# Optimization experiments

Measured on AMD Instinct MI355X. Metric: run time of the kernel, lower is better.

## Reference

```python
import jax, jax.numpy as jnp
import numpy as np

B, C, H, W = 8, 256, 64, 64


def setup_inputs() -> dict:
    key = jax.random.key(0)
    ks = jax.random.split(key, 6)
    s = 0.02
    return {
        "x": jax.random.normal(ks[0], (B, C, H, W), dtype=jnp.float32),
        "w_theta": jax.random.normal(ks[1], (C // 8, C), dtype=jnp.float32) * s,
        "b_theta": jnp.zeros((C // 8,), dtype=jnp.float32),
        "w_phi": jax.random.normal(ks[2], (C // 8, C), dtype=jnp.float32) * s,
        "b_phi": jnp.zeros((C // 8,), dtype=jnp.float32),
        "w_g": jax.random.normal(ks[3], (C // 2, C), dtype=jnp.float32) * s,
        "b_g": jnp.zeros((C // 2,), dtype=jnp.float32),
        "w_o": jax.random.normal(ks[4], (C, C // 2), dtype=jnp.float32) * s,
        "b_o": jnp.zeros((C,), dtype=jnp.float32),
        "gamma": jnp.zeros((1,), dtype=jnp.float32),
    }


def _conv1x1(x, w, b):
    # x: [B,Cin,H,W], w: [Cout,Cin] -> [B,Cout,H,W]
    return jnp.einsum('bchw,oc->bohw', x, w) + b[None, :, None, None]


def _maxpool2(t):
    b, c, h, w = t.shape
    return t.reshape(b, c, h // 2, 2, w // 2, 2).max(axis=(3, 5))


def reference(x, w_theta, b_theta, w_phi, b_phi, w_g, b_g, w_o, b_o, gamma):
    b, c, h, w = x.shape
    theta = _conv1x1(x, w_theta, b_theta).reshape(b, c // 8, h * w)      # [B,C/8,HW]
    phi = _maxpool2(_conv1x1(x, w_phi, b_phi)).reshape(b, c // 8, h * w // 4)  # [B,C/8,HW/4]
    attn = jax.nn.softmax(jnp.einsum('bcn,bcm->bnm', theta, phi), axis=-1)    # [B,HW,HW/4]
    g = _maxpool2(_conv1x1(x, w_g, b_g)).reshape(b, c // 2, h * w // 4)       # [B,C/2,HW/4]
    o = jnp.einsum('bcm,bnm->bcn', g, attn).reshape(b, c // 2, h, w)          # [B,C/2,H,W]
    o = _conv1x1(o, w_o, b_o)
    return gamma * o + x
```

## Files before the change

kernel.cpp:

```cpp
#include <hip/hip_runtime.h>
#include <cstdint>
#include <cstddef>

#define BATCH 8
#define CIN   256
#define CK    32
#define CV    128
#define HW_   4096
#define HWP   1024

typedef __attribute__((ext_vector_type(8))) short bf16x8;
typedef __attribute__((ext_vector_type(4))) float f32x4;
typedef __attribute__((ext_vector_type(4))) short short4v;

__device__ __forceinline__ short f2bf(float f) {
    union { float f; unsigned u; } v; v.f = f;
    unsigned r = v.u + 0x7fffu + ((v.u >> 16) & 1u);
    return (short)(r >> 16);
}
__device__ __forceinline__ float bf2f(short s) {
    union { unsigned u; float f; } v; v.u = ((unsigned)(unsigned short)s) << 16;
    return v.f;
}

#define WCAT_OFF 0u
#define WO_OFF   98304u
#define BCAT_OFF 163840u
#define XT_OFF   164864u
#define THT_OFF  16942080u
#define PHIT_OFF 19039232u
#define GP_OFF   19563520u

__global__ void prep_kernel(const float* __restrict__ wt, const float* __restrict__ bt,
                            const float* __restrict__ wp, const float* __restrict__ bp,
                            const float* __restrict__ wg, const float* __restrict__ bg,
                            const float* __restrict__ wo,
                            short* __restrict__ wcat_b, float* __restrict__ bcat,
                            short* __restrict__ wo_b) {
    int idx = blockIdx.x * 256 + threadIdx.x;
    if (idx < 192 * 256) {
        int o = idx >> 8, c = idx & 255;
        float v;
        if (o < 32)      v = wt[o * CIN + c];
        else if (o < 64) v = wp[(o - 32) * CIN + c];
        else             v = wg[(o - 64) * CIN + c];
        wcat_b[idx] = f2bf(v);
    } else {
        int i2 = idx - 192 * 256;
        wo_b[i2] = f2bf(wo[i2]);
    }
    if (blockIdx.x == 0 && threadIdx.x < 192) {
        int o = threadIdx.x;
        bcat[o] = (o < 32) ? bt[o] : (o < 64) ? bp[o - 32] : bg[o - 64];
    }
}

__global__ void __launch_bounds__(256) xt_kernel(const float* __restrict__ x,
                                                 short* __restrict__ x_t) {
    __shared__ float xs[64][65];
    int blk = blockIdx.x;
    int b = blk >> 8, rem = blk & 255, cblk = rem >> 6, nblk = rem & 63;
    int t = threadIdx.x;
#pragma unroll
    for (int i = 0; i < 16; ++i) {
        int idx = t + i * 256, c = idx >> 6, n = idx & 63;
        xs[c][n] = x[((size_t)(b * CIN + cblk * 64 + c)) * HW_ + nblk * 64 + n];
    }
    __syncthreads();
#pragma unroll
    for (int i = 0; i < 16; ++i) {
        int idx = t + i * 256, n = idx >> 6, c = idx & 63;
        x_t[((size_t)(b * HW_ + nblk * 64 + n)) * CIN + cblk * 64 + c] = f2bf(xs[c][n]);
    }
}

__global__ void __launch_bounds__(512) proj_pool_kernel(const short* __restrict__ x_t,
                                                        const short* __restrict__ wcat_b,
                                                        const float* __restrict__ bcat,
                                                        short* __restrict__ theta_t,
                                                        short* __restrict__ phi_t,
                                                        short* __restrict__ g_p) {
    __shared__ __align__(16) char smem[65536];
    int id = blockIdx.x;
    int b = id >> 5, rp = id & 31;
    int n0 = rp * 128;
    int t = threadIdx.x, l = t & 63, w = t >> 6, l15 = l & 15, lg = l >> 4;

#pragma unroll
    for (int i = 0; i < 8; ++i) {
        int chunk = t + i * 512, n = chunk >> 5, cc = chunk & 31;
        bf16x8 v = *(const bf16x8*)(x_t + ((size_t)(b * HW_ + n0 + n)) * CIN + cc * 8);
        *(bf16x8*)(smem + n * 512 + ((cc * 16) ^ ((n & 7) << 4))) = v;
    }
    __syncthreads();

    int og = w >> 1, nh = w & 1;
    f32x4 acc[3][4];
#pragma unroll
    for (int a = 0; a < 3; ++a)
#pragma unroll
        for (int nt = 0; nt < 4; ++nt) acc[a][nt] = (f32x4)0.f;

    for (int kk = 0; kk < 8; ++kk) {
        bf16x8 ao[3], bn[4];
#pragma unroll
        for (int oi = 0; oi < 3; ++oi) {
            int orow = og * 48 + oi * 16 + l15;
            ao[oi] = *(const bf16x8*)(wcat_b + orow * CIN + kk * 32 + lg * 8);
        }
#pragma unroll
        for (int nt = 0; nt < 4; ++nt) {
            int nr = nh * 64 + nt * 16 + l15;
            bn[nt] = *(const bf16x8*)(smem + nr * 512 + ((kk * 64 + lg * 16) ^ ((nr & 7) << 4)));
        }
#pragma unroll
        for (int oi = 0; oi < 3; ++oi)
#pragma unroll
            for (int nt = 0; nt < 4; ++nt)
                acc[oi][nt] = __builtin_amdgcn_mfma_f32_16x16x32_bf16(ao[oi], bn[nt], acc[oi][nt], 0, 0, 0);
    }
    __syncthreads();

#pragma unroll
    for (int oi = 0; oi < 3; ++oi)
#pragma unroll
        for (int nt = 0; nt < 4; ++nt)
#pragma unroll
            for (int r = 0; r < 4; ++r) {
                int o = og * 48 + oi * 16 + lg * 4 + r;
                int n = nh * 64 + nt * 16 + l15;
                float val = acc[oi][nt][r] + bcat[o];
                if (o < 32) val *= 1.44269504f;
                *(short*)(smem + n * 384 + ((o * 2) ^ ((n & 7) << 4))) = f2bf(val);
            }
    __syncthreads();

    {
        int n = t >> 2, cc = t & 3;
        bf16x8 v = *(const bf16x8*)(smem + n * 384 + ((cc * 16) ^ ((n & 7) << 4)));
        *(bf16x8*)(theta_t + ((size_t)(b * HW_ + n0 + n)) * CK + cc * 8) = v;
    }
#pragma unroll
    for (int jj = 0; jj < 2; ++jj) {
        int idx = t + jj * 512, wp = idx >> 5, c = idx & 31, o = 32 + c;
        int na = 2 * wp, nb2 = 2 * wp + 1;
        float v0 = bf2f(*(const short*)(smem + na * 384 + ((o * 2) ^ ((na & 7) << 4))));
        float v1 = bf2f(*(const short*)(smem + nb2 * 384 + ((o * 2) ^ ((nb2 & 7) << 4))));
        float v2 = bf2f(*(const short*)(smem + (64 + na) * 384 + ((o * 2) ^ (((64 + na) & 7) << 4))));
        float v3 = bf2f(*(const short*)(smem + (64 + nb2) * 384 + ((o * 2) ^ (((64 + nb2) & 7) << 4))));
        phi_t[((size_t)(b * HWP + rp * 32 + wp)) * CK + c] = f2bf(fmaxf(fmaxf(v0, v1), fmaxf(v2, v3)));
    }
#pragma unroll
    for (int jj = 0; jj < 8; ++jj) {
        int idx = t + jj * 512, cv = idx >> 5, wp = idx & 31, o = 64 + cv;
        int na = 2 * wp, nb2 = 2 * wp + 1;
        float v0 = bf2f(*(const short*)(smem + na * 384 + ((o * 2) ^ ((na & 7) << 4))));
        float v1 = bf2f(*(const short*)(smem + nb2 * 384 + ((o * 2) ^ ((nb2 & 7) << 4))));
        float v2 = bf2f(*(const short*)(smem + (64 + na) * 384 + ((o * 2) ^ (((64 + na) & 7) << 4))));
        float v3 = bf2f(*(const short*)(smem + (64 + nb2) * 384 + ((o * 2) ^ (((64 + nb2) & 7) << 4))));
        g_p[((size_t)(b * CV + cv)) * HWP + rp * 32 + wp] = f2bf(fmaxf(fmaxf(v0, v1), fmaxf(v2, v3)));
    }
}

#define PHI_PITCH 80
#define APHI0 0
#define AG0   5120
#define APHI1 21504
#define AG1   26624
#define AP    43008
#define ALS   51200
#define ALINV 52224
#define AO    0

__global__ void __launch_bounds__(256) attn_out_kernel(const short* __restrict__ theta_t,
                                                       const short* __restrict__ phi_t,
                                                       const short* __restrict__ g_p,
                                                       const short* __restrict__ wo_b,
                                                       const float* __restrict__ b_o,
                                                       const float* __restrict__ gamma,
                                                       const float* __restrict__ x,
                                                       float* __restrict__ out) {
    __shared__ __align__(16) char smem[52480];
    int id = blockIdx.x;
    int b = id & 7, q = id >> 3;
    int n0 = q * 64;
    int t = threadIdx.x, w = t >> 6, l = t & 63, l15 = l & 15, lg = l >> 4;

    bf16x8 qb[4];
#pragma unroll
    for (int nt = 0; nt < 4; ++nt)
        qb[nt] = *(const bf16x8*)(theta_t + ((size_t)(b * HW_ + n0 + nt * 16 + l15)) * CK + lg * 8);

    f32x4 oacc[8];
#pragma unroll
    for (int i = 0; i < 8; ++i) oacc[i] = (f32x4)0.f;
    float l_part[4] = {0.f, 0.f, 0.f, 0.f};

    const int sphioff = (t >> 2) * PHI_PITCH + (t & 3) * 16;
    const short* phisrc = phi_t + ((size_t)(b * HWP + (t >> 2))) * CK + (t & 3) * 8;
    const int mc = t & 7, cvb = t >> 3;
    const short* gs0 = g_p + ((size_t)(b * CV + cvb)) * HWP + mc * 8;
    const short* gs1 = gs0 + (size_t)32 * HWP;
    const short* gs2 = gs0 + (size_t)64 * HWP;
    const short* gs3 = gs0 + (size_t)96 * HWP;
    const int sg0 = cvb * 128 + ((mc * 16) ^ ((cvb & 7) << 4));
    const int sg1 = (cvb + 32) * 128 + ((mc * 16) ^ (((cvb + 32) & 7) << 4));
    const int sg2 = (cvb + 64) * 128 + ((mc * 16) ^ (((cvb + 64) & 7) << 4));
    const int sg3 = (cvb + 96) * 128 + ((mc * 16) ^ (((cvb + 96) & 7) << 4));

    bf16x8 pphi = *(const bf16x8*)phisrc;
    bf16x8 pg0 = *(const bf16x8*)gs0, pg1 = *(const bf16x8*)gs1;
    bf16x8 pg2 = *(const bf16x8*)gs2, pg3 = *(const bf16x8*)gs3;
    *(bf16x8*)(smem + APHI0 + sphioff) = pphi;
    *(bf16x8*)(smem + AG0 + sg0) = pg0;
    *(bf16x8*)(smem + AG0 + sg1) = pg1;
    *(bf16x8*)(smem + AG0 + sg2) = pg2;
    *(bf16x8*)(smem + AG0 + sg3) = pg3;
    __syncthreads();

    for (int kt = 0; kt < 16; ++kt) {
        const int cur = kt & 1;
        const int sb_phi = cur ? APHI1 : APHI0;
        const int sb_g   = cur ? AG1 : AG0;
        if (kt < 15) {
            phisrc += 64 * CK; gs0 += 64; gs1 += 64; gs2 += 64; gs3 += 64;
            pphi = *(const bf16x8*)phisrc;
            pg0 = *(const bf16x8*)gs0; pg1 = *(const bf16x8*)gs1;
            pg2 = *(const bf16x8*)gs2; pg3 = *(const bf16x8*)gs3;
        }
        bf16x8 pa = *(const bf16x8*)(smem + sb_phi + (w * 16 + l15) * PHI_PITCH + lg * 16);
        f32x4 sacc[4];
#pragma unroll
        for (int nt = 0; nt < 4; ++nt)
            sacc[nt] = __builtin_amdgcn_mfma_f32_16x16x32_bf16(pa, qb[nt], (f32x4)0.f, 0, 0, 0);
#pragma unroll
        for (int nt = 0; nt < 4; ++nt) {
            float p0 = __builtin_amdgcn_exp2f(sacc[nt][0]);
            float p1 = __builtin_amdgcn_exp2f(sacc[nt][1]);
            float p2 = __builtin_amdgcn_exp2f(sacc[nt][2]);
            float p3 = __builtin_amdgcn_exp2f(sacc[nt][3]);
            l_part[nt] += (p0 + p1) + (p2 + p3);
            short4v pk;
            pk[0] = f2bf(p0); pk[1] = f2bf(p1); pk[2] = f2bf(p2); pk[3] = f2bf(p3);
            int n = nt * 16 + l15;
            *(short4v*)(smem + AP + n * 128 + ((w * 32 + lg * 8) ^ ((n & 7) << 4))) = pk;
        }
        __syncthreads();

#pragma unroll
        for (int ks = 0; ks < 2; ++ks) {
            int np = w * 16 + l15;
            bf16x8 pva = *(const bf16x8*)(smem + AP + np * 128 + ((ks * 64 + lg * 16) ^ ((np & 7) << 4)));
#pragma unroll
            for (int cvt = 0; cvt < 8; ++cvt) {
                int cv = cvt * 16 + l15;
                bf16x8 gb = *(const bf16x8*)(smem + sb_g + cv * 128 + ((ks * 64 + lg * 16) ^ ((cv & 7) << 4)));
                oacc[cvt] = __builtin_amdgcn_mfma_f32_16x16x32_bf16(pva, gb, oacc[cvt], 0, 0, 0);
            }
        }
        if (kt < 15) {
            const int nb_phi = cur ? APHI0 : APHI1;
            const int nb_g   = cur ? AG0 : AG1;
            *(bf16x8*)(smem + nb_phi + sphioff) = pphi;
            *(bf16x8*)(smem + nb_g + sg0) = pg0;
            *(bf16x8*)(smem + nb_g + sg1) = pg1;
            *(bf16x8*)(smem + nb_g + sg2) = pg2;
            *(bf16x8*)(smem + nb_g + sg3) = pg3;
        }
        __syncthreads();
    }

#pragma unroll
    for (int nt = 0; nt < 4; ++nt) {
        l_part[nt] += __shfl_xor(l_part[nt], 16);
        l_part[nt] += __shfl_xor(l_part[nt], 32);
    }
    if (lg == 0) {
#pragma unroll
        for (int nt = 0; nt < 4; ++nt)
            *(float*)(smem + ALS + (nt * 16 + l15) * 16 + w * 4) = l_part[nt];
    }
    __syncthreads();
    if (t < 64) {
        f32x4 s4 = *(const f32x4*)(smem + ALS + t * 16);
        *(float*)(smem + ALINV + t * 4) = 1.f / ((s4[0] + s4[1]) + (s4[2] + s4[3]));
    }
    __syncthreads();
    f32x4 linv = *(const f32x4*)(smem + ALINV + (w * 16 + lg * 4) * 4);

#pragma unroll
    for (int cvt = 0; cvt < 8; ++cvt)
#pragma unroll
        for (int r = 0; r < 4; ++r) {
            int n = w * 16 + lg * 4 + r, cv = cvt * 16 + l15;
            *(short*)(smem + AO + n * 256 + ((cv * 2) ^ ((n & 7) << 4))) = f2bf(oacc[cvt][r] * linv[r]);
        }
    __syncthreads();

    f32x4 acc2[4][4];
#pragma unroll
    for (int a = 0; a < 4; ++a)
#pragma unroll
        for (int nt = 0; nt < 4; ++nt) acc2[a][nt] = (f32x4)0.f;

    for (int kk = 0; kk < 4; ++kk) {
        bf16x8 wa[4], ob[4];
#pragma unroll
        for (int ot = 0; ot < 4; ++ot) {
            int orow = w * 64 + ot * 16 + l15;
            wa[ot] = *(const bf16x8*)(wo_b + orow * CV + kk * 32 + lg * 8);
        }
#pragma unroll
        for (int nt = 0; nt < 4; ++nt) {
            int nl = nt * 16 + l15;
            ob[nt] = *(const bf16x8*)(smem + AO + nl * 256 + ((kk * 64 + lg * 16) ^ ((nl & 7) << 4)));
        }
#pragma unroll
        for (int ot = 0; ot < 4; ++ot)
#pragma unroll
            for (int nt = 0; nt < 4; ++nt)
                acc2[ot][nt] = __builtin_amdgcn_mfma_f32_16x16x32_bf16(wa[ot], ob[nt], acc2[ot][nt], 0, 0, 0);
    }

    float gm = gamma[0];
#pragma unroll
    for (int ot = 0; ot < 4; ++ot)
#pragma unroll
        for (int r = 0; r < 4; ++r) {
            int o = w * 64 + ot * 16 + lg * 4 + r;
            float bo = b_o[o];
#pragma unroll
            for (int nt = 0; nt < 4; ++nt) {
                size_t idx = ((size_t)(b * CIN + o)) * HW_ + n0 + nt * 16 + l15;
                out[idx] = fmaf(gm, acc2[ot][nt][r] + bo, x[idx]);
            }
        }
}

extern "C" void kernel_launch(void* const* d_in, const int* in_sizes, int n_in,
                              void* d_out, int out_size, void* d_ws, size_t ws_size,
                              hipStream_t stream) {
    const float* x       = (const float*)d_in[0];
    const float* w_theta = (const float*)d_in[1];
    const float* b_theta = (const float*)d_in[2];
    const float* w_phi   = (const float*)d_in[3];
    const float* b_phi   = (const float*)d_in[4];
    const float* w_g     = (const float*)d_in[5];
    const float* b_g     = (const float*)d_in[6];
    const float* w_o     = (const float*)d_in[7];
    const float* b_o     = (const float*)d_in[8];
    const float* gamma   = (const float*)d_in[9];
    float* out = (float*)d_out;
    char* wsb = (char*)d_ws;

    short* wcat_b  = (short*)(wsb + WCAT_OFF);
    short* wo_b    = (short*)(wsb + WO_OFF);
    float* bcat    = (float*)(wsb + BCAT_OFF);
    short* x_t     = (short*)(wsb + XT_OFF);
    short* theta_t = (short*)(wsb + THT_OFF);
    short* phi_t   = (short*)(wsb + PHIT_OFF);
    short* g_p     = (short*)(wsb + GP_OFF);

    prep_kernel<<<dim3(320), dim3(256), 0, stream>>>(w_theta, b_theta, w_phi, b_phi,
                                                     w_g, b_g, w_o, wcat_b, bcat, wo_b);
    xt_kernel<<<dim3(2048), dim3(256), 0, stream>>>(x, x_t);
    proj_pool_kernel<<<dim3(256), dim3(512), 0, stream>>>(x_t, wcat_b, bcat,
                                                          theta_t, phi_t, g_p);
    attn_out_kernel<<<dim3(512), dim3(256), 0, stream>>>(theta_t, phi_t, g_p, wo_b,
                                                         b_o, gamma, x, out);
}
```

Before: 146.1 us.

## Fuse x transpose/bf16 conversion into projection kernel with double-buffered fp32 staging

Removes the separate xt_kernel, which transposed x into an HW-major bf16 workspace. The projection kernel now reads fp32 x directly in 32-channel slices and stages them in a swizzled, double-buffered LDS tile, prefetching the next slice into registers while the current one is used. It converts to bf16 while building the MFMA B operand. This drops one kernel launch and an 16 MB write plus read round trip. In exchange it adds scalar LDS reads and per-element conversion in the inner loop, and a barrier on every k-step.

```diff
diff --git a/kernel.cpp b/kernel.cpp
--- a/kernel.cpp
+++ b/kernel.cpp
@@ -26,7 +26,6 @@
 #define WCAT_OFF 0u
 #define WO_OFF   98304u
 #define BCAT_OFF 163840u
-#define XT_OFF   164864u
 #define THT_OFF  16942080u
 #define PHIT_OFF 19039232u
 #define GP_OFF   19563520u
@@ -55,43 +54,30 @@
     }
 }
 
-__global__ void __launch_bounds__(256) xt_kernel(const float* __restrict__ x,
-                                                 short* __restrict__ x_t) {
-    __shared__ float xs[64][65];
-    int blk = blockIdx.x;
-    int b = blk >> 8, rem = blk & 255, cblk = rem >> 6, nblk = rem & 63;
-    int t = threadIdx.x;
-#pragma unroll
-    for (int i = 0; i < 16; ++i) {
-        int idx = t + i * 256, c = idx >> 6, n = idx & 63;
-        xs[c][n] = x[((size_t)(b * CIN + cblk * 64 + c)) * HW_ + nblk * 64 + n];
-    }
-    __syncthreads();
-#pragma unroll
-    for (int i = 0; i < 16; ++i) {
-        int idx = t + i * 256, n = idx >> 6, c = idx & 63;
-        x_t[((size_t)(b * HW_ + nblk * 64 + n)) * CIN + cblk * 64 + c] = f2bf(xs[c][n]);
-    }
-}
-
-__global__ void __launch_bounds__(512) proj_pool_kernel(const short* __restrict__ x_t,
+#define XS_PITCH 528
+#define XS_SZ    16896
+__global__ void __launch_bounds__(512) proj_pool_kernel(const float* __restrict__ x,
                                                         const short* __restrict__ wcat_b,
                                                         const float* __restrict__ bcat,
                                                         short* __restrict__ theta_t,
                                                         short* __restrict__ phi_t,
                                                         short* __restrict__ g_p) {
-    __shared__ __align__(16) char smem[65536];
+    __shared__ __align__(16) char smem[49152];
     int id = blockIdx.x;
     int b = id >> 5, rp = id & 31;
     int n0 = rp * 128;
     int t = threadIdx.x, l = t & 63, w = t >> 6, l15 = l & 15, lg = l >> 4;
 
-#pragma unroll
-    for (int i = 0; i < 8; ++i) {
-        int chunk = t + i * 512, n = chunk >> 5, cc = chunk & 31;
-        bf16x8 v = *(const bf16x8*)(x_t + ((size_t)(b * HW_ + n0 + n)) * CIN + cc * 8);
-        *(bf16x8*)(smem + n * 512 + ((cc * 16) ^ ((n & 7) << 4))) = v;
-    }
+    const int cl = t >> 4, nb = (t & 15) * 8;
+    const int swz_w = ((cl >> 3) & 3) << 5;
+    const int wo0 = cl * XS_PITCH + ((nb * 4) ^ swz_w);
+    const int wo1 = cl * XS_PITCH + (((nb + 4) * 4) ^ swz_w);
+    const float* xsrc = x + ((size_t)(b * CIN + cl) * HW_ + n0 + nb);
+
+    f32x4 sa = *(const f32x4*)(xsrc);
+    f32x4 sb = *(const f32x4*)(xsrc + 4);
+    *(f32x4*)(smem + wo0) = sa;
+    *(f32x4*)(smem + wo1) = sb;
     __syncthreads();
 
     int og = w >> 1, nh = w & 1;
@@ -102,24 +88,42 @@
         for (int nt = 0; nt < 4; ++nt) acc[a][nt] = (f32x4)0.f;
 
     for (int kk = 0; kk < 8; ++kk) {
+        const int cur = kk & 1;
+        if (kk < 7) {
+            const float* nsrc = xsrc + (size_t)(kk + 1) * 32 * HW_;
+            sa = *(const f32x4*)(nsrc);
+            sb = *(const f32x4*)(nsrc + 4);
+        }
         bf16x8 ao[3], bn[4];
 #pragma unroll
         for (int oi = 0; oi < 3; ++oi) {
             int orow = og * 48 + oi * 16 + l15;
             ao[oi] = *(const bf16x8*)(wcat_b + orow * CIN + kk * 32 + lg * 8);
         }
-#pragma unroll
-        for (int nt = 0; nt < 4; ++nt) {
-            int nr = nh * 64 + nt * 16 + l15;
-            bn[nt] = *(const bf16x8*)(smem + nr * 512 + ((kk * 64 + lg * 16) ^ ((nr & 7) << 4)));
+        {
+            const char* xsb = smem + cur * XS_SZ + lg * (8 * XS_PITCH);
+#pragma unroll
+            for (int nt = 0; nt < 4; ++nt) {
+                const int nby = (((nh * 64 + nt * 16 + l15) * 4) ^ (lg << 5));
+                bf16x8 bv;
+#pragma unroll
+                for (int j = 0; j < 8; ++j)
+                    bv[j] = f2bf(*(const float*)(xsb + j * XS_PITCH + nby));
+                bn[nt] = bv;
+            }
         }
 #pragma unroll
         for (int oi = 0; oi < 3; ++oi)
 #pragma unroll
             for (int nt = 0; nt < 4; ++nt)
                 acc[oi][nt] = __builtin_amdgcn_mfma_f32_16x16x32_bf16(ao[oi], bn[nt], acc[oi][nt], 0, 0, 0);
-    }
-    __syncthreads();
+        if (kk < 7) {
+            char* d = smem + (cur ^ 1) * XS_SZ;
+            *(f32x4*)(d + wo0) = sa;
+            *(f32x4*)(d + wo1) = sb;
+        }
+        __syncthreads();
+    }
 
 #pragma unroll
     for (int oi = 0; oi < 3; ++oi)
@@ -356,15 +360,13 @@
     short* wcat_b  = (short*)(wsb + WCAT_OFF);
     short* wo_b    = (short*)(wsb + WO_OFF);
     float* bcat    = (float*)(wsb + BCAT_OFF);
-    short* x_t     = (short*)(wsb + XT_OFF);
     short* theta_t = (short*)(wsb + THT_OFF);
     short* phi_t   = (short*)(wsb + PHIT_OFF);
     short* g_p     = (short*)(wsb + GP_OFF);
 
     prep_kernel<<<dim3(320), dim3(256), 0, stream>>>(w_theta, b_theta, w_phi, b_phi,
                                                      w_g, b_g, w_o, wcat_b, bcat, wo_b);
-    xt_kernel<<<dim3(2048), dim3(256), 0, stream>>>(x, x_t);
-    proj_pool_kernel<<<dim3(256), dim3(512), 0, stream>>>(x_t, wcat_b, bcat,
+    proj_pool_kernel<<<dim3(256), dim3(512), 0, stream>>>(x, wcat_b, bcat,
                                                           theta_t, phi_t, g_p);
     attn_out_kernel<<<dim3(512), dim3(256), 0, stream>>>(theta_t, phi_t, g_p, wo_b,
                                                          b_o, gamma, x, out);
```

Result: faster. 141.2 us (-3.4%).
